# Kernel tuning notes

Measured on AMD Instinct MI355X. Metric: run time of the kernel, lower is better.

The kernel has to match this reference:

```python
import jax, jax.numpy as jnp
import numpy as np

B, N, C, H, PD, CLN = 8, 1024, 512, 8, 256, 64
HD = C // H
HID = 4 * C
LN_EPS = 1e-5
ATT_EPS = 1e-6


def layernorm(x, g, b):
    mu = x.mean(-1, keepdims=True)
    var = ((x - mu) ** 2).mean(-1, keepdims=True)
    return (x - mu) * jax.lax.rsqrt(var + LN_EPS) * g + b


def setup_inputs() -> dict:
    key = jax.random.key(0)
    ks = jax.random.split(key, 16)
    p = lambda k, shp, s=0.02: (jax.random.normal(k, shp, dtype=jnp.float32) * s)
    return {
        "x_token": jax.random.normal(ks[0], (B, N, C), dtype=jnp.float32),
        "x_path": jax.random.normal(ks[1], (B, N, PD), dtype=jnp.float32),
        "wq": p(ks[2], (C, C)),
        "wk": p(ks[3], (C, C)),
        "wv": p(ks[4], (C, C)),
        "w_proj": p(ks[5], (C, C)),
        "b_proj": jnp.zeros((C,), jnp.float32),
        "g1": jnp.ones((C,), jnp.float32),
        "b1": jnp.zeros((C,), jnp.float32),
        "g2": jnp.ones((C,), jnp.float32),
        "b2": jnp.zeros((C,), jnp.float32),
        "w1": p(ks[6], (HID, C)),
        "bb1": jnp.zeros((HID,), jnp.float32),
        "w2": p(ks[7], (C, HID)),
        "bb2": jnp.zeros((C,), jnp.float32),
        "idx_cluster": jax.random.randint(ks[8], (B, N), 0, CLN, dtype=jnp.int64 if jax.config.jax_enable_x64 else jnp.int32),
        "cluster_num": CLN,
    }


def reference(x_token, x_path, wq, wk, wv, w_proj, b_proj, g1, b1, g2, b2,
              w1, bb1, w2, bb2, idx_cluster, cluster_num):
    Bn, Nn, Cn = x_token.shape
    scale = (Cn // H) ** -0.5

    # norm1 + attention
    t = layernorm(x_token, g1, b1)
    q = (t @ wq.T).reshape(Bn, Nn, H, HD).transpose(0, 2, 1, 3)  # bhnd
    k = (t @ wk.T).reshape(Bn, Nn, H, HD).transpose(0, 2, 1, 3)
    v = (t @ wv.T).reshape(Bn, Nn, H, HD).transpose(0, 2, 1, 3)

    # scatter-to-(B,cluster,N,C) then sum over clusters == same-cluster mask on QK^T
    scores = jnp.einsum("bhid,bhjd->bhij", q, k) * scale  # (B,H,N,N)
    same = (idx_cluster[:, None, :, None] == idx_cluster[:, None, None, :])  # (B,1,N,N)
    scores = jnp.where(same, scores, jnp.float32(-1e9))

    # custom eps-stabilized exp-softmax (as in the torch code, no max-subtraction)
    e = jnp.exp(scores.astype(jnp.float32))
    attn = (e + ATT_EPS / Nn) / (e.sum(-1, keepdims=True) + ATT_EPS)

    out = jnp.einsum("bhij,bhjd->bhid", attn, v)
    out = out.transpose(0, 2, 1, 3).reshape(Bn, Nn, Cn)
    out = out @ w_proj.T + b_proj

    x = x_token + out  # drop_path is identity in eval

    # MLP block
    h = layernorm(x, g2, b2)
    m = jax.nn.gelu(h @ w1.T + bb1, approximate=False) @ w2.T + bb2
    return x + m
```

## Files before the change

kernel.cpp:

```cpp
#include <hip/hip_runtime.h>

typedef unsigned short u16;
typedef __attribute__((ext_vector_type(4))) float f32x4;
typedef __attribute__((ext_vector_type(8))) short s16x8;
typedef __attribute__((ext_vector_type(4))) unsigned short u16x4;
typedef __attribute__((ext_vector_type(8))) unsigned short u16x8;

__device__ __forceinline__ u16 f2bf(float f) {
    unsigned int u = __builtin_bit_cast(unsigned int, f);
    u += 0x7fffu + ((u >> 16) & 1u);
    return (u16)(u >> 16);
}
__device__ __forceinline__ float bf2f(u16 h) {
    unsigned int u = ((unsigned int)h) << 16;
    return __builtin_bit_cast(float, u);
}
__device__ __forceinline__ void gload16(const u16* g, u16* l) {
    __builtin_amdgcn_global_load_lds(
        (const __attribute__((address_space(1))) void*)g,
        (__attribute__((address_space(3))) void*)l, 16, 0, 0);
}

__global__ __launch_bounds__(256) void cvt_all(const float* __restrict__ wq,
                                               const float* __restrict__ wk,
                                               const float* __restrict__ wv,
                                               const float* __restrict__ wp,
                                               const float* __restrict__ w1,
                                               const float* __restrict__ w2,
                                               u16* __restrict__ dqkv,
                                               u16* __restrict__ dp,
                                               u16* __restrict__ dw1,
                                               u16* __restrict__ dw2,
                                               float* __restrict__ vsum) {
    int b = blockIdx.x;
    if (b >= 3072) {
        float4 z = {0.f, 0.f, 0.f, 0.f};
        ((float4*)vsum)[(b - 3072) * 256 + threadIdx.x] = z;
        return;
    }
    const float* src; u16* dst; int off;
    if      (b < 256)  { src = wq; dst = dqkv;          off = b; }
    else if (b < 512)  { src = wk; dst = dqkv + 262144; off = b - 256; }
    else if (b < 768)  { src = wv; dst = dqkv + 524288; off = b - 512; }
    else if (b < 1024) { src = wp; dst = dp;            off = b - 768; }
    else if (b < 2048) { src = w1; dst = dw1;           off = b - 1024; }
    else               { src = w2; dst = dw2;           off = b - 2048; }
    int i = off * 256 + threadIdx.x;
    float4 v = ((const float4*)src)[i];
    u16x4 o;
    o.x = f2bf(v.x); o.y = f2bf(v.y); o.z = f2bf(v.z); o.w = f2bf(v.w);
    ((u16x4*)dst)[i] = o;
}

__global__ __launch_bounds__(128) void ln_kernel(const float* __restrict__ in,
                                                 const float* __restrict__ g,
                                                 const float* __restrict__ bta,
                                                 u16* __restrict__ out) {
    int row = blockIdx.x;
    int t = threadIdx.x;
    float4 v = ((const float4*)(in + (size_t)row * 512))[t];
    float s  = v.x + v.y + v.z + v.w;
    float s2 = v.x * v.x + v.y * v.y + v.z * v.z + v.w * v.w;
#pragma unroll
    for (int m = 1; m < 64; m <<= 1) { s += __shfl_xor(s, m); s2 += __shfl_xor(s2, m); }
    __shared__ float sh[4];
    if ((t & 63) == 0) { sh[(t >> 6) * 2] = s; sh[(t >> 6) * 2 + 1] = s2; }
    __syncthreads();
    s = sh[0] + sh[2]; s2 = sh[1] + sh[3];
    float mu  = s * (1.0f / 512.0f);
    float var = s2 * (1.0f / 512.0f) - mu * mu;
    float rstd = rsqrtf(var + 1e-5f);
    float4 gv = ((const float4*)g)[t];
    float4 bv = ((const float4*)bta)[t];
    u16x4 o;
    o.x = f2bf((v.x - mu) * rstd * gv.x + bv.x);
    o.y = f2bf((v.y - mu) * rstd * gv.y + bv.y);
    o.z = f2bf((v.z - mu) * rstd * gv.z + bv.z);
    o.w = f2bf((v.w - mu) * rstd * gv.w + bv.w);
    ((u16x4*)(out + (size_t)row * 512))[t] = o;
}

__global__ __launch_bounds__(512) void vsum_part(const u16* __restrict__ qkv,
                                                 float* __restrict__ vsum) {
    int b = blockIdx.x >> 3, chunk = blockIdx.x & 7;
    int c = threadIdx.x;
    const u16* base = qkv + (size_t)b * 1024 * 1536 + 1024 + c;
    float s = 0.0f;
    for (int n = chunk * 128; n < chunk * 128 + 128; ++n) s += bf2f(base[(size_t)n * 1536]);
    atomicAdd(&vsum[b * 512 + c], s);
}

__global__ __launch_bounds__(1024) void cluster_sort(const int* __restrict__ idx,
                                                     int* __restrict__ perm,
                                                     int* __restrict__ cstart,
                                                     int* __restrict__ ccnt) {
    const int b = blockIdx.x, t = threadIdx.x;
    const int w = t >> 6, lane = t & 63;
    __shared__ int whist[16][64];
    __shared__ int cnt[64];
    __shared__ int off[64];
    ((int*)whist)[t] = 0;
    __syncthreads();
    const int myc = idx[b * 1024 + t];
    atomicAdd(&whist[w][myc], 1);
    int rank_w = 0;
    for (int c = 0; c < 64; ++c) {
        unsigned long long m = __ballot(myc == c);
        if (myc == c) rank_w = __popcll(m & ((1ull << lane) - 1ull));
    }
    __syncthreads();
    if (t < 64) {
        int s = 0;
        for (int ww = 0; ww < 16; ++ww) s += whist[ww][t];
        cnt[t] = s;
        ccnt[b * 64 + t] = s;
    }
    __syncthreads();
    if (t == 0) {
        int s = 0;
        for (int c = 0; c < 64; ++c) { off[c] = s; s += cnt[c]; }
    }
    __syncthreads();
    int cross = 0;
    for (int ww = 0; ww < w; ++ww) cross += whist[ww][myc];
    perm[b * 1024 + off[myc] + cross + rank_w] = t;
    if (t < 64) cstart[b * 64 + t] = off[t];
}

__global__ __launch_bounds__(64) void cattn_kernel(const u16* __restrict__ qkv,
                                                   const int* __restrict__ perm,
                                                   const int* __restrict__ cstart,
                                                   const int* __restrict__ ccnt,
                                                   const float* __restrict__ vsum,
                                                   u16* __restrict__ O) {
    const int bid = blockIdx.x;
    const int h = bid & 7, c = (bid >> 3) & 63, b = bid >> 9;
    const int m = ccnt[b * 64 + c];
    if (m == 0) return;
    const int start = b * 1024 + cstart[b * 64 + c];
    const int lane = threadIdx.x;
    const int fr = lane & 15, fkb = lane >> 4;
    __shared__ __align__(16) u16 Qs[16 * 72];
    __shared__ __align__(16) u16 Ks[32 * 72];
    __shared__ __align__(16) u16 Vt[64 * 36];
    __shared__ __align__(16) u16 Pl[16 * 40];

    const u16* qkv_b = qkv + (size_t)b * 1024 * 1536;
    const float epsN = 1e-6f / 1024.0f;

    for (int q0 = 0; q0 < m; q0 += 16) {
        __syncthreads();
        {
            int row = lane >> 3, seg = lane & 7;
#pragma unroll
            for (int p = 0; p < 2; ++p) {
                int r = row + p * 8;
                int gr = perm[start + min(q0 + r, m - 1)];
                *(int4*)(&Qs[r * 72 + seg * 8]) =
                    *(const int4*)(qkv_b + (size_t)gr * 1536 + h * 64 + seg * 8);
            }
        }
        __syncthreads();
        const s16x8 qf0 = *(const s16x8*)(&Qs[fr * 72 + fkb * 8]);
        const s16x8 qf1 = *(const s16x8*)(&Qs[fr * 72 + 32 + fkb * 8]);

        f32x4 oacc[4] = {};
        float rs[4] = {0.f, 0.f, 0.f, 0.f};

        for (int k0 = 0; k0 < m; k0 += 32) {
            __syncthreads();
            {
                int row = lane >> 3, seg = lane & 7;
#pragma unroll
                for (int p = 0; p < 4; ++p) {
                    int r = row + p * 8;
                    int gr = perm[start + min(k0 + r, m - 1)];
                    const u16* src = qkv_b + (size_t)gr * 1536 + h * 64 + seg * 8;
                    *(int4*)(&Ks[r * 72 + seg * 8]) = *(const int4*)(src + 512);
                    u16x8 vv = *(const u16x8*)(src + 1024);
#pragma unroll
                    for (int i = 0; i < 8; ++i) Vt[(seg * 8 + i) * 36 + r] = vv[i];
                }
            }
            __syncthreads();
#pragma unroll
            for (int ct = 0; ct < 2; ++ct) {
                f32x4 sacc = {};
                s16x8 kf0 = *(const s16x8*)(&Ks[(ct * 16 + fr) * 72 + fkb * 8]);
                s16x8 kf1 = *(const s16x8*)(&Ks[(ct * 16 + fr) * 72 + 32 + fkb * 8]);
                sacc = __builtin_amdgcn_mfma_f32_16x16x32_bf16(qf0, kf0, sacc, 0, 0, 0);
                sacc = __builtin_amdgcn_mfma_f32_16x16x32_bf16(qf1, kf1, sacc, 0, 0, 0);
                bool valid = (k0 + ct * 16 + fr) < m;
#pragma unroll
                for (int r = 0; r < 4; ++r) {
                    float e = valid ? __expf(sacc[r] * 0.125f) : 0.0f;
                    rs[r] += e;
                    Pl[(fkb * 4 + r) * 40 + ct * 16 + fr] = f2bf(e);
                }
            }
            __syncthreads();
            s16x8 pf = *(const s16x8*)(&Pl[fr * 40 + fkb * 8]);
#pragma unroll
            for (int dt = 0; dt < 4; ++dt) {
                s16x8 vf = *(const s16x8*)(&Vt[(dt * 16 + fr) * 36 + fkb * 8]);
                oacc[dt] = __builtin_amdgcn_mfma_f32_16x16x32_bf16(pf, vf, oacc[dt], 0, 0, 0);
            }
        }
#pragma unroll
        for (int r = 0; r < 4; ++r)
#pragma unroll
            for (int mm = 1; mm < 16; mm <<= 1) rs[r] += __shfl_xor(rs[r], mm);

#pragma unroll
        for (int r = 0; r < 4; ++r) {
            int ql = q0 + fkb * 4 + r;
            if (ql < m) {
                int orow = perm[start + ql];
#pragma unroll
                for (int dt = 0; dt < 4; ++dt) {
                    int dcol = dt * 16 + fr;
                    float vs = vsum[(b * 8 + h) * 64 + dcol];
                    float val = (oacc[dt][r] + epsN * vs) / (rs[r] + 1e-6f);
                    O[((size_t)(b * 1024 + orow)) * 512 + h * 64 + dcol] = f2bf(val);
                }
            }
        }
    }
}

template <int BM, bool OUT_BF16, bool BIAS, bool RESID, bool GELU>
__global__ __launch_bounds__(256) void gemm2p(const u16* __restrict__ A,
                                              const u16* __restrict__ W,
                                              const float* __restrict__ bias,
                                              const float* __restrict__ resid,
                                              void* __restrict__ outp,
                                              int M, int N, int K) {
    constexpr int MI = BM / 32;
    __shared__ __align__(16) u16 As[2][BM * 64];
    __shared__ __align__(16) u16 Bs[2][128 * 64];
    const int bm = blockIdx.x, bn = blockIdx.y;
    const int t = threadIdx.x;
    const int lane = t & 63, w = t >> 6;
    const int wm = w >> 1, wn = w & 1;
    const int fr = lane & 15, fkb = lane >> 4;
    const int l8 = lane >> 3;
    const int c8s = (((lane & 7) ^ (l8 & 7)) * 8);
    f32x4 acc[MI][4] = {};
    const u16* Ab = A + (size_t)bm * BM * K;
    const u16* Wb = W + (size_t)bn * 128 * K;
    const int nt = K >> 6;

#define STAGE(buf, k0)                                                            \
    {                                                                             \
        _Pragma("unroll") for (int j = 0; j < MI; ++j) {                          \
            int r = (w * MI + j) * 8 + l8;                                        \
            gload16(Ab + (size_t)r * K + (k0) + c8s, &As[buf][(w * MI + j) * 512]); \
        }                                                                         \
        _Pragma("unroll") for (int j = 0; j < 4; ++j) {                           \
            int r = (w * 4 + j) * 8 + l8;                                         \
            gload16(Wb + (size_t)r * K + (k0) + c8s, &Bs[buf][(w * 4 + j) * 512]); \
        }                                                                         \
    }

    STAGE(0, 0);
    __syncthreads();

    int cur = 0;
    for (int kt = 0; kt < nt; ++kt) {
        if (kt + 1 < nt) STAGE(cur ^ 1, (kt + 1) << 6);
#pragma unroll
        for (int kk = 0; kk < 64; kk += 32) {
            s16x8 af[MI], bfv[4];
#pragma unroll
            for (int mi = 0; mi < MI; ++mi) {
                int R = wm * (BM / 2) + mi * 16 + fr;
                int off = R * 64 + ((((kk >> 3) + fkb) ^ (fr & 7)) << 3);
                af[mi] = *(const s16x8*)(&As[cur][off]);
            }
#pragma unroll
            for (int ni = 0; ni < 4; ++ni) {
                int R = wn * 64 + ni * 16 + fr;
                int off = R * 64 + ((((kk >> 3) + fkb) ^ (fr & 7)) << 3);
                bfv[ni] = *(const s16x8*)(&Bs[cur][off]);
            }
#pragma unroll
            for (int mi = 0; mi < MI; ++mi)
#pragma unroll
                for (int ni = 0; ni < 4; ++ni)
                    acc[mi][ni] = __builtin_amdgcn_mfma_f32_16x16x32_bf16(
                        af[mi], bfv[ni], acc[mi][ni], 0, 0, 0);
        }
        __syncthreads();
        cur ^= 1;
    }
#undef STAGE

    const int rg = (lane >> 4) * 4;
#pragma unroll
    for (int mi = 0; mi < MI; ++mi) {
#pragma unroll
        for (int ni = 0; ni < 4; ++ni) {
            int gcol = bn * 128 + wn * 64 + ni * 16 + fr;
            float bv = BIAS ? bias[gcol] : 0.0f;
#pragma unroll
            for (int r = 0; r < 4; ++r) {
                int grow = bm * BM + wm * (BM / 2) + mi * 16 + rg + r;
                float v = acc[mi][ni][r] + bv;
                if (GELU) v = 0.5f * v * (1.0f + erff(v * 0.70710678118f));
                if (RESID) v += resid[(size_t)grow * N + gcol];
                if (OUT_BF16)
                    ((u16*)outp)[(size_t)grow * N + gcol] = f2bf(v);
                else
                    ((float*)outp)[(size_t)grow * N + gcol] = v;
            }
        }
    }
}

extern "C" void kernel_launch(void* const* d_in, const int* in_sizes, int n_in,
                              void* d_out, int out_size, void* d_ws, size_t ws_size,
                              hipStream_t stream) {
    const float* x_token = (const float*)d_in[0];
    const float* wq     = (const float*)d_in[2];
    const float* wk     = (const float*)d_in[3];
    const float* wv     = (const float*)d_in[4];
    const float* w_proj = (const float*)d_in[5];
    const float* b_proj = (const float*)d_in[6];
    const float* g1     = (const float*)d_in[7];
    const float* b1     = (const float*)d_in[8];
    const float* g2     = (const float*)d_in[9];
    const float* b2     = (const float*)d_in[10];
    const float* w1     = (const float*)d_in[11];
    const float* bb1    = (const float*)d_in[12];
    const float* w2     = (const float*)d_in[13];
    const float* bb2    = (const float*)d_in[14];
    const int*   idx    = (const int*)d_in[15];
    float* out_f = (float*)d_out;

    char* ws = (char*)d_ws;
    u16*   t_buf = (u16*)(ws);
    u16*   qkv   = (u16*)(ws + 8388608);
    u16*   Obuf  = (u16*)(ws + 8388608 + 25165824);
    u16*   m1    = qkv;
    float* xbuf  = (float*)(ws + 41943040);
    u16*   h_buf = t_buf;
    char*  wsw   = ws + 58720256;
    u16*   wqkv  = (u16*)(wsw);
    u16*   wprjb = (u16*)(wsw + 1572864);
    u16*   w1b   = (u16*)(wsw + 2097152);
    u16*   w2b   = (u16*)(wsw + 4194304);
    float* vsum  = (float*)(wsw + 6291456);
    int*   perm   = (int*)xbuf;
    int*   cstart = (int*)((char*)xbuf + 32768);
    int*   ccnt   = (int*)((char*)xbuf + 34816);
    (void)ws_size; (void)in_sizes; (void)n_in; (void)out_size;

    cvt_all<<<3076, 256, 0, stream>>>(wq, wk, wv, w_proj, w1, w2,
                                      wqkv, wprjb, w1b, w2b, vsum);
    cluster_sort<<<8, 1024, 0, stream>>>(idx, perm, cstart, ccnt);

    ln_kernel<<<8192, 128, 0, stream>>>(x_token, g1, b1, t_buf);
    gemm2p<128, true, false, false, false><<<dim3(64, 12), 256, 0, stream>>>(
        t_buf, wqkv, nullptr, nullptr, qkv, 8192, 1536, 512);
    vsum_part<<<64, 512, 0, stream>>>(qkv, vsum);
    cattn_kernel<<<4096, 64, 0, stream>>>(qkv, perm, cstart, ccnt, vsum, Obuf);
    gemm2p<64, false, true, true, false><<<dim3(128, 4), 256, 0, stream>>>(
        Obuf, wprjb, b_proj, x_token, xbuf, 8192, 512, 512);
    ln_kernel<<<8192, 128, 0, stream>>>(xbuf, g2, b2, h_buf);
    gemm2p<128, true, true, false, true><<<dim3(64, 16), 256, 0, stream>>>(
        h_buf, w1b, bb1, nullptr, m1, 8192, 2048, 512);
    gemm2p<64, false, true, true, false><<<dim3(128, 4), 256, 0, stream>>>(
        m1, w2b, bb2, xbuf, out_f, 8192, 512, 2048);
}
```

Baseline: 159.4 us.

## Use 256x256-tile 8-wave GEMM with split-K atomics for MLP down-projection

Adds a 512-thread GEMM kernel with 256x256 output tiles and 8 waves, each computing a 128x64 sub-tile, to raise reuse per LDS load. It replaces the QKV and fc1 GEMMs. The fc2 GEMM (K=2048) is now split-K across 4 z-slices and accumulates into the output with float atomics. A separate init kernel first writes residual plus bias into the output. The larger tiles give fewer blocks (192/256/256 grids) and add register pressure, and the atomic accumulation makes float summation order nondeterministic and adds atomic traffic.

```diff
diff --git a/kernel.cpp b/kernel.cpp
--- a/kernel.cpp
+++ b/kernel.cpp
@@ -88,6 +88,16 @@
     float s = 0.0f;
     for (int n = chunk * 128; n < chunk * 128 + 128; ++n) s += bf2f(base[(size_t)n * 1536]);
     atomicAdd(&vsum[b * 512 + c], s);
+}
+
+__global__ __launch_bounds__(256) void init_out(const float* __restrict__ x,
+                                                const float* __restrict__ bb2,
+                                                float* __restrict__ out) {
+    int i = blockIdx.x * 256 + threadIdx.x;
+    float4 v = ((const float4*)x)[i];
+    float4 b = ((const float4*)bb2)[i & 127];
+    v.x += b.x; v.y += b.y; v.z += b.z; v.w += b.w;
+    ((float4*)out)[i] = v;
 }
 
 __global__ __launch_bounds__(1024) void cluster_sort(const int* __restrict__ idx,
@@ -222,6 +232,99 @@
                     float vs = vsum[(b * 8 + h) * 64 + dcol];
                     float val = (oacc[dt][r] + epsN * vs) / (rs[r] + 1e-6f);
                     O[((size_t)(b * 1024 + orow)) * 512 + h * 64 + dcol] = f2bf(val);
+                }
+            }
+        }
+    }
+}
+
+template <bool OUT_BF16, bool BIAS, bool GELU, bool ATOMIC>
+__global__ __launch_bounds__(512, 2) void gemm8w(const u16* __restrict__ A,
+                                                 const u16* __restrict__ W,
+                                                 const float* __restrict__ bias,
+                                                 void* __restrict__ outp,
+                                                 int N, int LDK, int KS) {
+    __shared__ __align__(16) u16 As[2][256 * 64];
+    __shared__ __align__(16) u16 Bs[2][256 * 64];
+    const int bm = blockIdx.x, bn = blockIdx.y;
+    const int t = threadIdx.x;
+    const int lane = t & 63, w = t >> 6;
+    const int wm = w >> 2, wn = w & 3;
+    const int fr = lane & 15, fkb = lane >> 4;
+    const int l8 = lane >> 3;
+    const int c8s = (((lane & 7) ^ (l8 & 7)) * 8);
+    const int kbase = blockIdx.z * KS;
+    f32x4 acc[8][4] = {};
+    const u16* Ab = A + (size_t)bm * 256 * LDK + kbase;
+    const u16* Wb = W + (size_t)bn * 256 * LDK + kbase;
+    const int nt = KS >> 6;
+
+#define STAGE8(buf, k0)                                                            \
+    {                                                                              \
+        _Pragma("unroll") for (int j = 0; j < 4; ++j) {                            \
+            int rr = (w * 4 + j) * 8 + l8;                                         \
+            gload16(Ab + (size_t)rr * LDK + (k0) + c8s, &As[buf][(w * 4 + j) * 512]); \
+            gload16(Wb + (size_t)rr * LDK + (k0) + c8s, &Bs[buf][(w * 4 + j) * 512]); \
+        }                                                                          \
+    }
+
+    STAGE8(0, 0);
+
+    int cur = 0;
+    for (int kt = 0; kt < nt; ++kt) {
+        if (kt + 1 < nt) {
+            STAGE8(cur ^ 1, (kt + 1) << 6);
+            __builtin_amdgcn_sched_barrier(0);
+            asm volatile("s_waitcnt vmcnt(8)" ::: "memory");
+        } else {
+            asm volatile("s_waitcnt vmcnt(0)" ::: "memory");
+        }
+        __builtin_amdgcn_sched_barrier(0);
+        __builtin_amdgcn_s_barrier();
+        __builtin_amdgcn_sched_barrier(0);
+#pragma unroll
+        for (int kk = 0; kk < 64; kk += 32) {
+            const int co = (((kk >> 3) + fkb) ^ (fr & 7)) << 3;
+            s16x8 af[8], bfv[4];
+#pragma unroll
+            for (int mi = 0; mi < 8; ++mi)
+                af[mi] = *(const s16x8*)(&As[cur][(wm * 128 + mi * 16 + fr) * 64 + co]);
+#pragma unroll
+            for (int ni = 0; ni < 4; ++ni)
+                bfv[ni] = *(const s16x8*)(&Bs[cur][(wn * 64 + ni * 16 + fr) * 64 + co]);
+#pragma unroll
+            for (int mi = 0; mi < 8; ++mi)
+#pragma unroll
+                for (int ni = 0; ni < 4; ++ni)
+                    acc[mi][ni] = __builtin_amdgcn_mfma_f32_16x16x32_bf16(
+                        af[mi], bfv[ni], acc[mi][ni], 0, 0, 0);
+        }
+        asm volatile("s_waitcnt lgkmcnt(0)" ::: "memory");
+        __builtin_amdgcn_sched_barrier(0);
+        __builtin_amdgcn_s_barrier();
+        __builtin_amdgcn_sched_barrier(0);
+        cur ^= 1;
+    }
+#undef STAGE8
+
+    const int rg = (lane >> 4) * 4;
+#pragma unroll
+    for (int mi = 0; mi < 8; ++mi) {
+#pragma unroll
+        for (int ni = 0; ni < 4; ++ni) {
+            int gcol = bn * 256 + wn * 64 + ni * 16 + fr;
+            float bv = BIAS ? bias[gcol] : 0.0f;
+#pragma unroll
+            for (int r = 0; r < 4; ++r) {
+                int grow = bm * 256 + wm * 128 + mi * 16 + rg + r;
+                float v = acc[mi][ni][r] + bv;
+                if (GELU) v = 0.5f * v * (1.0f + erff(v * 0.70710678118f));
+                if (ATOMIC) {
+                    atomicAdd((float*)outp + (size_t)grow * N + gcol, v);
+                } else if (OUT_BF16) {
+                    ((u16*)outp)[(size_t)grow * N + gcol] = f2bf(v);
+                } else {
+                    ((float*)outp)[(size_t)grow * N + gcol] = v;
                 }
             }
         }
@@ -360,15 +463,16 @@
     cluster_sort<<<8, 1024, 0, stream>>>(idx, perm, cstart, ccnt);
 
     ln_kernel<<<8192, 128, 0, stream>>>(x_token, g1, b1, t_buf);
-    gemm2p<128, true, false, false, false><<<dim3(64, 12), 256, 0, stream>>>(
-        t_buf, wqkv, nullptr, nullptr, qkv, 8192, 1536, 512);
+    gemm8w<true, false, false, false><<<dim3(32, 6, 1), 512, 0, stream>>>(
+        t_buf, wqkv, nullptr, qkv, 1536, 512, 512);
     vsum_part<<<64, 512, 0, stream>>>(qkv, vsum);
     cattn_kernel<<<4096, 64, 0, stream>>>(qkv, perm, cstart, ccnt, vsum, Obuf);
     gemm2p<64, false, true, true, false><<<dim3(128, 4), 256, 0, stream>>>(
         Obuf, wprjb, b_proj, x_token, xbuf, 8192, 512, 512);
     ln_kernel<<<8192, 128, 0, stream>>>(xbuf, g2, b2, h_buf);
-    gemm2p<128, true, true, false, true><<<dim3(64, 16), 256, 0, stream>>>(
-        h_buf, w1b, bb1, nullptr, m1, 8192, 2048, 512);
-    gemm2p<64, false, true, true, false><<<dim3(128, 4), 256, 0, stream>>>(
-        m1, w2b, bb2, xbuf, out_f, 8192, 512, 2048);
-}
+    gemm8w<true, true, true, false><<<dim3(32, 8, 1), 512, 0, stream>>>(
+        h_buf, w1b, bb1, m1, 2048, 512, 512);
+    init_out<<<4096, 256, 0, stream>>>(xbuf, bb2, out_f);
+    gemm8w<false, false, false, true><<<dim3(32, 2, 4), 512, 0, stream>>>(
+        m1, w2b, nullptr, out_f, 512, 2048, 512);
+}
```

Result: slower. 199.4 us (+25.0%).

## Replace double-buffered GEMM pipeline with single-buffered LDS staging

Applied to the files above, without the earlier changes.

The GEMM kernel drops its double-buffered LDS prefetch. Each 64-wide K tile is now loaded into a single buffer between two barriers and then consumed. This halves LDS use per block, which may allow more resident blocks per CU, but it gives up overlap between global-to-LDS loads and MFMA compute within a block.

```diff
diff --git a/kernel.cpp b/kernel.cpp
--- a/kernel.cpp
+++ b/kernel.cpp
@@ -229,15 +229,15 @@
 }
 
 template <int BM, bool OUT_BF16, bool BIAS, bool RESID, bool GELU>
-__global__ __launch_bounds__(256) void gemm2p(const u16* __restrict__ A,
-                                              const u16* __restrict__ W,
-                                              const float* __restrict__ bias,
-                                              const float* __restrict__ resid,
-                                              void* __restrict__ outp,
-                                              int M, int N, int K) {
+__global__ __launch_bounds__(256) void gemm_sb(const u16* __restrict__ A,
+                                               const u16* __restrict__ W,
+                                               const float* __restrict__ bias,
+                                               const float* __restrict__ resid,
+                                               void* __restrict__ outp,
+                                               int M, int N, int K) {
     constexpr int MI = BM / 32;
-    __shared__ __align__(16) u16 As[2][BM * 64];
-    __shared__ __align__(16) u16 Bs[2][128 * 64];
+    __shared__ __align__(16) u16 As[BM * 64];
+    __shared__ __align__(16) u16 Bs[128 * 64];
     const int bm = blockIdx.x, bn = blockIdx.y;
     const int t = threadIdx.x;
     const int lane = t & 63, w = t >> 6;
@@ -248,41 +248,30 @@
     f32x4 acc[MI][4] = {};
     const u16* Ab = A + (size_t)bm * BM * K;
     const u16* Wb = W + (size_t)bn * 128 * K;
-    const int nt = K >> 6;
-
-#define STAGE(buf, k0)                                                            \
-    {                                                                             \
-        _Pragma("unroll") for (int j = 0; j < MI; ++j) {                          \
-            int r = (w * MI + j) * 8 + l8;                                        \
-            gload16(Ab + (size_t)r * K + (k0) + c8s, &As[buf][(w * MI + j) * 512]); \
-        }                                                                         \
-        _Pragma("unroll") for (int j = 0; j < 4; ++j) {                           \
-            int r = (w * 4 + j) * 8 + l8;                                         \
-            gload16(Wb + (size_t)r * K + (k0) + c8s, &Bs[buf][(w * 4 + j) * 512]); \
-        }                                                                         \
-    }
-
-    STAGE(0, 0);
-    __syncthreads();
-
-    int cur = 0;
-    for (int kt = 0; kt < nt; ++kt) {
-        if (kt + 1 < nt) STAGE(cur ^ 1, (kt + 1) << 6);
+
+    for (int k0 = 0; k0 < K; k0 += 64) {
+        __syncthreads();
+#pragma unroll
+        for (int j = 0; j < MI; ++j) {
+            int r = (w * MI + j) * 8 + l8;
+            gload16(Ab + (size_t)r * K + k0 + c8s, &As[(w * MI + j) * 512]);
+        }
+#pragma unroll
+        for (int j = 0; j < 4; ++j) {
+            int r = (w * 4 + j) * 8 + l8;
+            gload16(Wb + (size_t)r * K + k0 + c8s, &Bs[(w * 4 + j) * 512]);
+        }
+        __syncthreads();
 #pragma unroll
         for (int kk = 0; kk < 64; kk += 32) {
+            const int co = (((kk >> 3) + fkb) ^ (fr & 7)) << 3;
             s16x8 af[MI], bfv[4];
 #pragma unroll
-            for (int mi = 0; mi < MI; ++mi) {
-                int R = wm * (BM / 2) + mi * 16 + fr;
-                int off = R * 64 + ((((kk >> 3) + fkb) ^ (fr & 7)) << 3);
-                af[mi] = *(const s16x8*)(&As[cur][off]);
-            }
-#pragma unroll
-            for (int ni = 0; ni < 4; ++ni) {
-                int R = wn * 64 + ni * 16 + fr;
-                int off = R * 64 + ((((kk >> 3) + fkb) ^ (fr & 7)) << 3);
-                bfv[ni] = *(const s16x8*)(&Bs[cur][off]);
-            }
+            for (int mi = 0; mi < MI; ++mi)
+                af[mi] = *(const s16x8*)(&As[(wm * (BM / 2) + mi * 16 + fr) * 64 + co]);
+#pragma unroll
+            for (int ni = 0; ni < 4; ++ni)
+                bfv[ni] = *(const s16x8*)(&Bs[(wn * 64 + ni * 16 + fr) * 64 + co]);
 #pragma unroll
             for (int mi = 0; mi < MI; ++mi)
 #pragma unroll
@@ -290,10 +279,7 @@
                     acc[mi][ni] = __builtin_amdgcn_mfma_f32_16x16x32_bf16(
                         af[mi], bfv[ni], acc[mi][ni], 0, 0, 0);
         }
-        __syncthreads();
-        cur ^= 1;
-    }
-#undef STAGE
+    }
 
     const int rg = (lane >> 4) * 4;
 #pragma unroll
@@ -360,15 +346,15 @@
     cluster_sort<<<8, 1024, 0, stream>>>(idx, perm, cstart, ccnt);
 
     ln_kernel<<<8192, 128, 0, stream>>>(x_token, g1, b1, t_buf);
-    gemm2p<128, true, false, false, false><<<dim3(64, 12), 256, 0, stream>>>(
+    gemm_sb<128, true, false, false, false><<<dim3(64, 12), 256, 0, stream>>>(
         t_buf, wqkv, nullptr, nullptr, qkv, 8192, 1536, 512);
     vsum_part<<<64, 512, 0, stream>>>(qkv, vsum);
     cattn_kernel<<<4096, 64, 0, stream>>>(qkv, perm, cstart, ccnt, vsum, Obuf);
-    gemm2p<64, false, true, true, false><<<dim3(128, 4), 256, 0, stream>>>(
+    gemm_sb<64, false, true, true, false><<<dim3(128, 4), 256, 0, stream>>>(
         Obuf, wprjb, b_proj, x_token, xbuf, 8192, 512, 512);
     ln_kernel<<<8192, 128, 0, stream>>>(xbuf, g2, b2, h_buf);
-    gemm2p<128, true, true, false, true><<<dim3(64, 16), 256, 0, stream>>>(
+    gemm_sb<128, true, true, false, true><<<dim3(64, 16), 256, 0, stream>>>(
         h_buf, w1b, bb1, nullptr, m1, 8192, 2048, 512);
-    gemm2p<64, false, true, true, false><<<dim3(128, 4), 256, 0, stream>>>(
+    gemm_sb<64, false, true, true, false><<<dim3(128, 4), 256, 0, stream>>>(
         m1, w2b, bb2, xbuf, out_f, 8192, 512, 2048);
 }
```

Measured after the change: 156.2 us. 1.02x faster.
